# Performance work log

Hardware: AMD Instinct MI355X
Metric: run time of the kernel (lower is better)

The kernel has to match this reference:

```python
import jax, jax.numpy as jnp
import numpy as np

# Dimensions inferred from VSSBlockOneWay(hidden_dim=256, ssm_d_state=64, forward_type='m0_noz')
B_, L_, D_ = 8, 2048, 256      # batch, seq_len, d_model
DIN, N_, P_ = 512, 64, 64      # d_inner = 2*d_model, d_state, head_dim
H_ = DIN // P_                 # n_heads = 8


def _ln(x, w, b, eps=1e-5):
    m = x.mean(-1, keepdims=True)
    v = ((x - m) ** 2).mean(-1, keepdims=True)
    return (x - m) * jax.lax.rsqrt(v + eps) * w + b


def setup_inputs() -> dict:
    key = jax.random.key(0)
    ks = jax.random.split(key, 8)
    s = lambda k, shape, sc: jax.random.normal(k, shape, jnp.float32) * sc
    return dict(
        src=jax.random.normal(ks[0], (B_, L_, D_), jnp.float32),
        ln_w=jnp.ones((D_,), jnp.float32), ln_b=jnp.zeros((D_,), jnp.float32),
        W_in=s(ks[1], (D_, DIN), 0.02),
        conv_w=s(ks[2], (DIN, 1, 3), 0.1),            # depthwise conv1d kernel
        conv_b=jnp.zeros((DIN,), jnp.float32),
        W_xproj=s(ks[3], (DIN, H_ + 2 * N_), 0.02),   # -> (dt | B | C)
        dt_bias=s(ks[4], (H_,), 0.1),
        A_log=jnp.log(jnp.arange(1, H_ + 1, dtype=jnp.float32)),  # Mamba2 A-init
        Ds=jnp.ones((H_,), jnp.float32),
        oln_w=jnp.ones((DIN,), jnp.float32), oln_b=jnp.zeros((DIN,), jnp.float32),
        W_out=s(ks[5], (DIN, D_), 0.02),
    )


def reference(src, ln_w, ln_b, W_in, conv_w, conv_b, W_xproj, dt_bias,
              A_log, Ds, oln_w, oln_b, W_out):
    B, L, D = src.shape
    H, N, P = H_, N_, P_
    x = _ln(src, ln_w, ln_b)
    u = x @ W_in                                                    # (B,L,DIN)
    # depthwise conv over sequence, SAME padding (VMamba uses non-causal dwconv)
    uc = jax.lax.conv_general_dilated(
        u.transpose(0, 2, 1), conv_w, (1,), 'SAME',
        feature_group_count=DIN, dimension_numbers=('NCH', 'OIH', 'NCH'))
    u = jax.nn.gelu((uc + conv_b[None, :, None]).transpose(0, 2, 1),
                    approximate=False)                              # (B,L,DIN)
    dbc = u @ W_xproj                                               # (B,L,H+2N)
    dt = jax.nn.softplus(dbc[..., :H] + dt_bias)                    # (B,L,H)
    Bm = dbc[..., H:H + N]                                          # (B,L,N)
    Cm = dbc[..., H + N:]                                           # (B,L,N)
    A = -jnp.exp(A_log)                                             # (H,)
    decay = jnp.exp(dt * A)                                         # (B,L,H)
    xh = u.reshape(B, L, H, P)
    dtx = dt[..., None] * xh                                        # (B,L,H,P)

    def step(h, inp):
        dec_t, dtx_t, B_t, C_t = inp
        # h: (B,H,P,N)
        h = h * dec_t[:, :, None, None] + dtx_t[..., None] * B_t[:, None, None, :]
        y = jnp.einsum('bhpn,bn->bhp', h, C_t)
        return h, y

    h0 = jnp.zeros((B, H, P, N), u.dtype)
    inputs = (decay.transpose(1, 0, 2), dtx.transpose(1, 0, 2, 3),
              Bm.transpose(1, 0, 2), Cm.transpose(1, 0, 2))
    _, ys = jax.lax.scan(step, h0, inputs)                          # (L,B,H,P)
    y = ys.transpose(1, 0, 2, 3) + xh * Ds[None, None, :, None]
    y = _ln(y.reshape(B, L, DIN), oln_w, oln_b)
    # dropout / drop_path are identity at inference
    return src + y @ W_out
```

## Files before the change

### kernel.cpp

```cpp
#include <hip/hip_runtime.h>
#include <hip/hip_bf16.h>
#include <cmath>

typedef __hip_bfloat16 bf16;
typedef short bf16x8 __attribute__((ext_vector_type(8)));
typedef short bf16x4v __attribute__((ext_vector_type(4)));
typedef float f32x4 __attribute__((ext_vector_type(4)));

constexpr int B_ = 8, L_ = 2048, D_ = 256, DIN_ = 512;
constexpr int H_ = 8, N_ = 64, P_ = 64;
constexpr int BL_ = B_ * L_;
constexpr int NCH_ = 136;
constexpr int Q_ = 64;
constexpr int NC_ = L_ / Q_;

static __device__ __forceinline__ float b2f(bf16 x) { return __bfloat162float(x); }
static __device__ __forceinline__ bf16  f2b(float x) { return __float2bfloat16(x); }
static __device__ __forceinline__ bf16  rawb(short s) { __hip_bfloat16_raw r; r.x = (unsigned short)s; return (bf16)r; }
static __device__ __forceinline__ float sane(float v) { return (fabsf(v) <= 1e30f) ? v : 0.f; }
static __device__ __forceinline__ float loadx(const void* p, size_t i, bool isbf) {
    return isbf ? b2f(((const bf16*)p)[i]) : ((const float*)p)[i];
}
static __device__ __forceinline__ bf16x8 load8x(const void* p, size_t off, bool isbf) {
    if (isbf) return *(const bf16x8*)((const bf16*)p + off);
    const float4* fp = (const float4*)((const float*)p + off);
    float4 f0 = fp[0], f1 = fp[1];
    bf16 t[8] = {f2b(f0.x), f2b(f0.y), f2b(f0.z), f2b(f0.w),
                 f2b(f1.x), f2b(f1.y), f2b(f1.z), f2b(f1.w)};
    return *(bf16x8*)t;
}
static __device__ __forceinline__ int swz(int row, int col) { return col ^ (((row >> 3) & 7) * 8); }

static __device__ __forceinline__ f32x4 mfma16(bf16x8 a, bf16x8 b, f32x4 c) {
    return __builtin_amdgcn_mfma_f32_16x16x32_bf16(a, b, c, 0, 0, 0);
}
#define ONES8 bf16x8{16256, 16256, 16256, 16256, 16256, 16256, 16256, 16256}

__global__ __launch_bounds__(256) void prep_k(const void* __restrict__ Win, const void* __restrict__ Wx,
                       const void* __restrict__ Wo,
                       const void* __restrict__ ln_w, const void* __restrict__ ln_b,
                       const void* __restrict__ oln_w, const void* __restrict__ oln_b,
                       bf16* __restrict__ WinT, bf16* __restrict__ WxT, bf16* __restrict__ WoT,
                       float* __restrict__ colsum1, float* __restrict__ bias1,
                       float* __restrict__ colsum2, float* __restrict__ bias2,
                       const unsigned short* __restrict__ flagp) {
    const bool isbf = flagp[0] != 0;
    const int bx = blockIdx.x, tid = threadIdx.x;
    if (bx < 88) {
        __shared__ float T[64][65];
        if (bx < 32) {
            int d0 = (bx & 3) * 64, n0 = (bx >> 2) * 64;
#pragma unroll
            for (int i = 0; i < 16; i++) {
                int e = tid + 256 * i; int r = e >> 6, c = e & 63;
                T[r][c] = loadx(Win, (size_t)(d0 + r) * DIN_ + n0 + c, isbf);
            }
            __syncthreads();
#pragma unroll
            for (int i = 0; i < 16; i++) {
                int e = tid + 256 * i; int r = e >> 6, c = e & 63;
                WinT[(size_t)(n0 + r) * D_ + d0 + c] = f2b(loadx(ln_w, d0 + c, isbf) * T[c][r]);
            }
        } else if (bx < 64) {
            int t2 = bx - 32;
            int k0 = (t2 & 7) * 64, d0 = (t2 >> 3) * 64;
#pragma unroll
            for (int i = 0; i < 16; i++) {
                int e = tid + 256 * i; int r = e >> 6, c = e & 63;
                T[r][c] = loadx(Wo, (size_t)(k0 + r) * D_ + d0 + c, isbf);
            }
            __syncthreads();
#pragma unroll
            for (int i = 0; i < 16; i++) {
                int e = tid + 256 * i; int r = e >> 6, c = e & 63;
                WoT[(size_t)(d0 + r) * DIN_ + k0 + c] = f2b(loadx(oln_w, k0 + c, isbf) * T[c][r]);
            }
        } else {
            int t3 = bx - 64;
            int i0 = (t3 & 7) * 64, j0 = (t3 >> 3) * 64;
#pragma unroll
            for (int i = 0; i < 16; i++) {
                int e = tid + 256 * i; int r = e >> 6, c = e & 63;
                int j = j0 + c;
                T[r][c] = (j < NCH_) ? loadx(Wx, (size_t)(i0 + r) * NCH_ + j, isbf) : 0.f;
            }
            __syncthreads();
#pragma unroll
            for (int i = 0; i < 16; i++) {
                int e = tid + 256 * i; int r = e >> 6, c = e & 63;
                WxT[(size_t)(j0 + r) * DIN_ + i0 + c] = f2b(T[c][r]);
            }
        }
        return;
    }
    const int o = (bx - 88) * 4 + (tid >> 6);
    const int lane = tid & 63;
    float cs = 0.f, bs = 0.f;
    if (o < DIN_) {
        int n = o;
        for (int i = lane; i < D_; i += 64) {
            float wv = loadx(Win, (size_t)i * DIN_ + n, isbf);
            cs += loadx(ln_w, i, isbf) * wv;
            bs += loadx(ln_b, i, isbf) * wv;
        }
    } else {
        int d = o - DIN_;
        for (int k = lane; k < DIN_; k += 64) {
            float wv = loadx(Wo, (size_t)k * D_ + d, isbf);
            cs += loadx(oln_w, k, isbf) * wv;
            bs += loadx(oln_b, k, isbf) * wv;
        }
    }
#pragma unroll
    for (int off = 32; off >= 1; off >>= 1) { cs += __shfl_xor(cs, off); bs += __shfl_xor(bs, off); }
    if (lane == 0) {
        if (o < DIN_) { colsum1[o] = cs; bias1[o] = bs; }
        else          { colsum2[o - DIN_] = cs; bias2[o - DIN_] = bs; }
    }
}

__global__ __launch_bounds__(256) void gemm1_k(const void* __restrict__ src,
                                               const bf16* __restrict__ WinT,
                                               const float* __restrict__ colsum1,
                                               const float* __restrict__ bias1,
                                               bf16* __restrict__ u0,
                                               const unsigned short* __restrict__ flagp) {
    const bool isbf = flagp[0] != 0;
    constexpr int K = D_;
    constexpr int STR = K + 8;
    constexpr int CH = K / 8;
    __shared__ bf16 Blds[64 * STR];
    const int tid = threadIdx.x;
    const int n0 = blockIdx.y * 64;
#pragma unroll
    for (int i = 0; i < 64 * CH / 256; i++) {
        int e = tid + 256 * i;
        int r = e / CH, cch = e % CH;
        bf16x8 v = *(const bf16x8*)(WinT + (size_t)(n0 + r) * K + cch * 8);
        *(bf16x8*)(&Blds[r * STR + cch * 8]) = v;
    }
    __syncthreads();
    const int wave = tid >> 6, lane = tid & 63;
    const int quad = lane >> 4, l16 = lane & 15;
    const int m0 = blockIdx.x * 128 + wave * 32;
    const bf16x8 ones = ONES8;
    f32x4 acc[2][4], accS[2], accS2[2];
#pragma unroll
    for (int i = 0; i < 2; i++) {
        accS[i] = f32x4{0.f, 0.f, 0.f, 0.f};
        accS2[i] = f32x4{0.f, 0.f, 0.f, 0.f};
#pragma unroll
        for (int j = 0; j < 4; j++) acc[i][j] = f32x4{0.f, 0.f, 0.f, 0.f};
    }
    const size_t r0 = (size_t)(m0 + l16) * K + quad * 8;
    const size_t r1 = r0 + (size_t)16 * K;
#pragma unroll
    for (int k0 = 0; k0 < K; k0 += 32) {
        bf16x8 a0 = load8x(src, r0 + k0, isbf);
        bf16x8 a1 = load8x(src, r1 + k0, isbf);
        accS[0]  = mfma16(a0, ones, accS[0]);
        accS2[0] = mfma16(a0, a0, accS2[0]);
        accS[1]  = mfma16(a1, ones, accS[1]);
        accS2[1] = mfma16(a1, a1, accS2[1]);
#pragma unroll
        for (int i = 0; i < 4; i++) {
            bf16x8 bb = *(const bf16x8*)(&Blds[(16 * i + l16) * STR + k0 + quad * 8]);
            acc[0][i] = mfma16(a0, bb, acc[0][i]);
            acc[1][i] = mfma16(a1, bb, acc[1][i]);
        }
    }
    float cs[4], bsv[4];
#pragma unroll
    for (int i = 0; i < 4; i++) { int n = n0 + 16 * i + l16; cs[i] = colsum1[n]; bsv[i] = bias1[n]; }
#pragma unroll
    for (int rb = 0; rb < 2; rb++)
#pragma unroll
        for (int r = 0; r < 4; r++) {
            int rl = quad * 4 + r;
            float sv  = accS[rb][r];
            float s2v = __shfl(accS2[rb][r], (quad << 4) + rl);
            float mean = sv * (1.f / D_);
            float var  = s2v * (1.f / D_) - mean * mean;
            float rs = rsqrtf(fmaxf(var, 0.f) + 1e-5f);
            int m = m0 + rb * 16 + rl;
#pragma unroll
            for (int i = 0; i < 4; i++) {
                int n = n0 + 16 * i + l16;
                float v = rs * (acc[rb][i][r] - mean * cs[i]) + bsv[i];
                u0[(size_t)m * DIN_ + n] = f2b(v);
            }
        }
}

template<int MODE>
__global__ __launch_bounds__(256) void gemmB_k(const bf16* __restrict__ A,
                                               const bf16* __restrict__ BT,
                                               void* __restrict__ Cout,
                                               const void* __restrict__ resid,
                                               const float* __restrict__ colsum,
                                               const float* __restrict__ biasv,
                                               const void* __restrict__ dt_bias,
                                               const void* __restrict__ A_log,
                                               float* __restrict__ dtg,
                                               float* __restrict__ dtAg,
                                               const unsigned short* __restrict__ flagp) {
    const bool isbf = flagp[0] != 0;
    constexpr int K = 512;
    constexpr int KH = 256;
    constexpr int STR = KH + 8;
    constexpr int CH = KH / 8;
    __shared__ bf16 Blds[64 * STR];
    const int tid = threadIdx.x;
    const int n0 = blockIdx.y * 64;
    const int wave = tid >> 6, lane = tid & 63;
    const int quad = lane >> 4, l16 = lane & 15;
    const int m0 = blockIdx.x * 128 + wave * 32;
    const bf16x8 ones = ONES8;
    f32x4 acc[2][4], accS[2], accS2[2];
#pragma unroll
    for (int i = 0; i < 2; i++) {
        accS[i] = f32x4{0.f, 0.f, 0.f, 0.f};
        accS2[i] = f32x4{0.f, 0.f, 0.f, 0.f};
#pragma unroll
        for (int j = 0; j < 4; j++) acc[i][j] = f32x4{0.f, 0.f, 0.f, 0.f};
    }
    const bf16* a0p = A + (size_t)(m0 + l16) * K + quad * 8;
    const bf16* a1p = a0p + (size_t)16 * K;
#pragma unroll
    for (int kh = 0; kh < 2; kh++) {
        if (kh) __syncthreads();
#pragma unroll
        for (int i = 0; i < 64 * CH / 256; i++) {
            int e = tid + 256 * i;
            int r = e / CH, cch = e % CH;
            bf16x8 v = *(const bf16x8*)(BT + (size_t)(n0 + r) * K + kh * KH + cch * 8);
            *(bf16x8*)(&Blds[r * STR + cch * 8]) = v;
        }
        __syncthreads();
        const bf16* ah0 = a0p + kh * KH;
        const bf16* ah1 = a1p + kh * KH;
#pragma unroll 4
        for (int k0 = 0; k0 < KH; k0 += 32) {
            bf16x8 a0 = *(const bf16x8*)(ah0 + k0);
            bf16x8 a1 = *(const bf16x8*)(ah1 + k0);
            if (MODE == 1) {
                accS[0]  = mfma16(a0, ones, accS[0]);
                accS2[0] = mfma16(a0, a0, accS2[0]);
                accS[1]  = mfma16(a1, ones, accS[1]);
                accS2[1] = mfma16(a1, a1, accS2[1]);
            }
#pragma unroll
            for (int i = 0; i < 4; i++) {
                bf16x8 bb = *(const bf16x8*)(&Blds[(16 * i + l16) * STR + k0 + quad * 8]);
                acc[0][i] = mfma16(a0, bb, acc[0][i]);
                acc[1][i] = mfma16(a1, bb, acc[1][i]);
            }
        }
    }
    if (MODE == 0) {
#pragma unroll
        for (int rb = 0; rb < 2; rb++)
#pragma unroll
            for (int r = 0; r < 4; r++) {
                int m = m0 + rb * 16 + quad * 4 + r;
#pragma unroll
                for (int i = 0; i < 4; i++) {
                    int n = n0 + 16 * i + l16;
                    if (n < NCH_) ((bf16*)Cout)[(size_t)m * NCH_ + n] = f2b(acc[rb][i][r]);
                }
            }
        if (blockIdx.y == 0 && l16 < 8) {
            float bb = loadx(dt_bias, l16, isbf);
            float Ah = -__expf(fminf(loadx(A_log, l16, isbf), 30.f));
#pragma unroll
            for (int rb = 0; rb < 2; rb++)
#pragma unroll
                for (int r = 0; r < 4; r++) {
                    int m = m0 + rb * 16 + quad * 4 + r;
                    float raw = acc[rb][0][r] + bb;
                    float sp = raw > 20.f ? raw : log1pf(__expf(raw));
                    sp = fminf(sp, 60.f);
                    dtg[(size_t)m * H_ + l16]  = sp;
                    dtAg[(size_t)m * H_ + l16] = sp * Ah;
                }
        }
    } else {
        float cs[4], bsv[4];
#pragma unroll
        for (int i = 0; i < 4; i++) { int n = n0 + 16 * i + l16; cs[i] = colsum[n]; bsv[i] = biasv[n]; }
#pragma unroll
        for (int rb = 0; rb < 2; rb++)
#pragma unroll
            for (int r = 0; r < 4; r++) {
                int rl = quad * 4 + r;
                float sv  = accS[rb][r];
                float s2v = __shfl(accS2[rb][r], (quad << 4) + rl);
                float mean = sv * (1.f / K);
                float var  = s2v * (1.f / K) - mean * mean;
                float rs = rsqrtf(fmaxf(var, 0.f) + 1e-5f);
                int m = m0 + rb * 16 + rl;
#pragma unroll
                for (int i = 0; i < 4; i++) {
                    int n = n0 + 16 * i + l16;
                    size_t o = (size_t)m * D_ + n;
                    float v = rs * (acc[rb][i][r] - mean * cs[i]) + bsv[i] + loadx(resid, o, isbf);
                    v = sane(v);
                    if (isbf) ((bf16*)Cout)[o] = f2b(v);
                    else      ((float*)Cout)[o] = v;
                }
            }
    }
}

constexpr int CSTRIP_ = 4;
__global__ __launch_bounds__(256) void conv_k(const bf16* __restrict__ u0,
                                              const void* __restrict__ cw,
                                              const void* __restrict__ cb,
                                              bf16* __restrict__ u,
                                              const unsigned short* __restrict__ flagp) {
    const bool isbf = flagp[0] != 0;
    __shared__ float wlds[2048];
    {
        int t = threadIdx.x;
#pragma unroll
        for (int i = 0; i < 6; i++) { int e = t + 256 * i; wlds[e] = loadx(cw, e, isbf); }
        wlds[t + 1536] = loadx(cb, t, isbf);
        wlds[t + 1792] = loadx(cb, t + 256, isbf);
    }
    __syncthreads();
    const int wave = threadIdx.x >> 6, lane = threadIdx.x & 63;
    const int sid = blockIdx.x * 4 + wave;
    const int bl0 = sid * CSTRIP_;
    const int l0 = bl0 & (L_ - 1);
    const int c8 = lane * 8;
    float w0[8], w1[8], w2[8], bias[8];
#pragma unroll
    for (int t = 0; t < 8; t++) {
        int ch = c8 + t;
        w0[t] = wlds[ch * 3 + 0];
        w1[t] = wlds[ch * 3 + 1];
        w2[t] = wlds[ch * 3 + 2];
        bias[t] = wlds[1536 + ch];
    }
    const bf16x8* rp = (const bf16x8*)(u0 + (size_t)bl0 * DIN_ + c8);
    bf16x8 zero = {0, 0, 0, 0, 0, 0, 0, 0};
    bf16x8 vl = (l0 > 0) ? rp[-64] : zero;
    bf16x8 vm = rp[0];
#pragma unroll
    for (int i = 0; i < CSTRIP_; i++) {
        int l = l0 + i;
        bf16x8 vr = (l < L_ - 1) ? rp[64 * (i + 1)] : zero;
        bf16 ob[8];
#pragma unroll
        for (int t = 0; t < 8; t++) {
            float a = bias[t] + w1[t] * b2f(rawb(vm[t]))
                    + w0[t] * b2f(rawb(vl[t])) + w2[t] * b2f(rawb(vr[t]));
            float ge = 0.5f * a * (1.f + erff(a * 0.70710678118f));
            ob[t] = f2b(ge);
        }
        *(bf16x8*)(u + (size_t)(bl0 + i) * DIN_ + c8) = *(bf16x8*)ob;
        vl = vm; vm = vr;
    }
}

__global__ __launch_bounds__(256) void chunk_state_k(const bf16* __restrict__ ubuf,
                                                     const bf16* __restrict__ dbcb,
                                                     const float* __restrict__ dtg,
                                                     const float* __restrict__ dtAg,
                                                     bf16* __restrict__ HS,
                                                     float* __restrict__ cdg) {
    const int idx = blockIdx.x;
    const int c = idx & 31, h = (idx >> 5) & 7, b = idx >> 8;
    const int bh = b * 8 + h;
    const int blbase = b * L_ + c * Q_;
    __shared__ bf16 Xw[64][72];
    __shared__ bf16 BTb[64][72];
    const int tid = threadIdx.x;
    const int lane = tid & 63;
    float dA  = dtAg[(size_t)(blbase + lane) * H_ + h];
    float dtv = dtg[(size_t)(blbase + lane) * H_ + h];
    const int jr = tid >> 3, p8 = (tid & 7) * 8;
    bf16x8 xv0 = *(const bf16x8*)(ubuf + (size_t)(blbase + jr) * DIN_ + h * 64 + p8);
    bf16x8 bv0 = *(const bf16x8*)(dbcb + (size_t)(blbase + jr) * NCH_ + 8 + p8);
    bf16x8 xv1 = *(const bf16x8*)(ubuf + (size_t)(blbase + jr + 32) * DIN_ + h * 64 + p8);
    bf16x8 bv1 = *(const bf16x8*)(dbcb + (size_t)(blbase + jr + 32) * NCH_ + 8 + p8);
    float v = dA;
#pragma unroll
    for (int off = 1; off < 64; off <<= 1) { float t = __shfl_up(v, off); if (lane >= off) v += t; }
    float segEnd = __shfl(v, 63);
    float fjl = __expf(fminf(segEnd - v, 0.f)) * dtv;
    if (tid == 0) cdg[bh * NC_ + c] = __expf(fminf(segEnd, 0.f));
    float fs0 = __shfl(fjl, jr);
    float fs1 = __shfl(fjl, jr + 32);
#pragma unroll
    for (int t = 0; t < 8; t++) {
        int p = p8 + t;
        Xw[p][swz(p, jr)]       = f2b(fs0 * b2f(rawb(xv0[t])));
        BTb[p][swz(p, jr)]      = rawb(bv0[t]);
        Xw[p][swz(p, jr + 32)]  = f2b(fs1 * b2f(rawb(xv1[t])));
        BTb[p][swz(p, jr + 32)] = rawb(bv1[t]);
    }
    __syncthreads();
    const int wave = tid >> 6, quad = lane >> 4, l16 = lane & 15;
    const int p0 = wave * 16;
    f32x4 acc[4];
#pragma unroll
    for (int i = 0; i < 4; i++) acc[i] = f32x4{0.f, 0.f, 0.f, 0.f};
#pragma unroll
    for (int ks = 0; ks < 2; ks++) {
        int pa = p0 + l16;
        bf16x8 a = *(const bf16x8*)(&Xw[pa][swz(pa, ks * 32 + quad * 8)]);
#pragma unroll
        for (int nt = 0; nt < 4; nt++) {
            int nb = nt * 16 + l16;
            bf16x8 bb = *(const bf16x8*)(&BTb[nb][swz(nb, ks * 32 + quad * 8)]);
            acc[nt] = mfma16(a, bb, acc[nt]);
        }
    }
    size_t slot = (size_t)(bh * NC_ + c) * 4096;
#pragma unroll
    for (int nt = 0; nt < 4; nt++)
#pragma unroll
        for (int r = 0; r < 4; r++) {
            int p = p0 + quad * 4 + r, n = nt * 16 + l16;
            HS[slot + p * 64 + n] = f2b(sane(acc[nt][r]));
        }
}

__global__ __launch_bounds__(256) void chunk_rec_k(bf16* __restrict__ HS,
                                                   const float* __restrict__ cdg) {
    const int bh = blockIdx.x >> 2, sub = blockIdx.x & 3;
    const int eo = sub * 1024 + threadIdx.x * 4;
    bf16* base = HS + (size_t)bh * (NC_ * 4096) + eo;
    bf16x4v v[NC_];
#pragma unroll
    for (int c = 0; c < NC_; c++) v[c] = *(const bf16x4v*)(base + (size_t)c * 4096);
    float cdr[NC_];
#pragma unroll
    for (int c = 0; c < NC_; c++) cdr[c] = cdg[bh * NC_ + c];
    float h0 = 0.f, h1 = 0.f, h2 = 0.f, h3 = 0.f;
#pragma unroll
    for (int c = 0; c < NC_; c++) {
        bf16 ob[4] = {f2b(h0), f2b(h1), f2b(h2), f2b(h3)};
        *(bf16x4v*)(base + (size_t)c * 4096) = *(bf16x4v*)ob;
        float cd = cdr[c];
        h0 = cd * h0 + b2f(rawb(v[c][0]));
        h1 = cd * h1 + b2f(rawb(v[c][1]));
        h2 = cd * h2 + b2f(rawb(v[c][2]));
        h3 = cd * h3 + b2f(rawb(v[c][3]));
    }
}

__global__ __launch_bounds__(256) void chunk_out_k(bf16* __restrict__ ubuf,
                                                   const bf16* __restrict__ dbcb,
                                                   const float* __restrict__ dtg,
                                                   const float* __restrict__ dtAg,
                                                   const bf16* __restrict__ HS,
                                                   const void* __restrict__ Ds,
                                                   bf16* __restrict__ ybuf,
                                                   const unsigned short* __restrict__ flagp) {
    const bool isbf = flagp[0] != 0;
    const int idx = blockIdx.x;
    const int c = idx & 31, h = (idx >> 5) & 7, b = idx >> 8;
    const int bh = b * 8 + h;
    const int blbase = b * L_ + c * Q_;
    const size_t slotbase = (size_t)(bh * NC_ + c) * 4096;
    __shared__ bf16 Xb[64][72];
    __shared__ bf16 Gb[64][72];
    const int tid = threadIdx.x;
    const int lane = tid & 63;
    float dA  = dtAg[(size_t)(blbase + lane) * H_ + h];
    float dtl = dtg[(size_t)(blbase + lane) * H_ + h];
    const int rr = tid >> 3, k8 = (tid & 7) * 8;
    bf16x8 xva = *(const bf16x8*)(ubuf + (size_t)(blbase + rr) * DIN_ + h * 64 + k8);
    bf16x8 xvb = *(const bf16x8*)(ubuf + (size_t)(blbase + rr + 32) * DIN_ + h * 64 + k8);
    float segl = dA;
#pragma unroll
    for (int off = 1; off < 64; off <<= 1) { float t = __shfl_up(segl, off); if (lane >= off) segl += t; }
    float PLl = __expf(fminf(segl, 0.f));
#pragma unroll
    for (int t = 0; t < 8; t++) {
        int p = k8 + t;
        Xb[p][swz(p, rr)]      = rawb(xva[t]);
        Xb[p][swz(p, rr + 32)] = rawb(xvb[t]);
    }
    __syncthreads();
    const int wave = tid >> 6, quad = lane >> 4, l16 = lane & 15;
    const int l0 = wave * 16;
    f32x4 g[4];
#pragma unroll
    for (int i = 0; i < 4; i++) g[i] = f32x4{0.f, 0.f, 0.f, 0.f};
#pragma unroll
    for (int ks = 0; ks < 2; ks++) {
        bf16x8 a = *(const bf16x8*)(dbcb + (size_t)(blbase + l0 + l16) * NCH_ + 72 + ks * 32 + quad * 8);
#pragma unroll
        for (int jt = 0; jt < 4; jt++) {
            bf16x8 bb = *(const bf16x8*)(dbcb + (size_t)(blbase + jt * 16 + l16) * NCH_ + 8 + ks * 32 + quad * 8);
            g[jt] = mfma16(a, bb, g[jt]);
        }
    }
#pragma unroll
    for (int jt = 0; jt < 4; jt++) {
        int j = jt * 16 + l16;
        float segj = __shfl(segl, j);
        float dtj  = __shfl(dtl, j);
#pragma unroll
        for (int r = 0; r < 4; r++) {
            int l = l0 + quad * 4 + r;
            float e = __expf(fminf(__shfl(segl, l) - segj, 0.f));
            float gv = (j <= l) ? sane(g[jt][r]) * e * dtj : 0.f;
            Gb[l][swz(l, j)] = f2b(sane(gv));
        }
    }
    __syncthreads();
    f32x4 y1[4], y2[4];
#pragma unroll
    for (int i = 0; i < 4; i++) { y1[i] = f32x4{0.f, 0.f, 0.f, 0.f}; y2[i] = f32x4{0.f, 0.f, 0.f, 0.f}; }
#pragma unroll
    for (int ks = 0; ks < 2; ks++) {
        int la = l0 + l16;
        bf16x8 ag = *(const bf16x8*)(&Gb[la][swz(la, ks * 32 + quad * 8)]);
        bf16x8 ac = *(const bf16x8*)(dbcb + (size_t)(blbase + la) * NCH_ + 72 + ks * 32 + quad * 8);
#pragma unroll
        for (int pt = 0; pt < 4; pt++) {
            int pb = pt * 16 + l16;
            bf16x8 bx = *(const bf16x8*)(&Xb[pb][swz(pb, ks * 32 + quad * 8)]);
            bf16x8 bhf = *(const bf16x8*)(HS + slotbase + (size_t)pb * 64 + ks * 32 + quad * 8);
            y1[pt] = mfma16(ag, bx, y1[pt]);
            y2[pt] = mfma16(ac, bhf, y2[pt]);
        }
    }
    float dsH = loadx(Ds, h, isbf);
#pragma unroll
    for (int pt = 0; pt < 4; pt++) {
        int p = pt * 16 + l16;
#pragma unroll
        for (int r = 0; r < 4; r++) {
            int l = l0 + quad * 4 + r;
            float yv = y1[pt][r] + __shfl(PLl, l) * y2[pt][r] + dsH * b2f(Xb[p][swz(p, l)]);
            ybuf[(size_t)(blbase + l) * DIN_ + h * 64 + p] = f2b(sane(yv));
        }
    }
}

extern "C" void kernel_launch(void* const* d_in, const int* in_sizes, int n_in,
                              void* d_out, int out_size, void* d_ws, size_t ws_size,
                              hipStream_t stream) {
    const void* src     = d_in[0];
    const void* ln_w    = d_in[1];
    const void* ln_b    = d_in[2];
    const void* W_in    = d_in[3];
    const void* conv_w  = d_in[4];
    const void* conv_b  = d_in[5];
    const void* W_xproj = d_in[6];
    const void* dt_bias = d_in[7];
    const void* A_log   = d_in[8];
    const void* Ds      = d_in[9];
    const void* oln_w   = d_in[10];
    const void* oln_b   = d_in[11];
    const void* W_out   = d_in[12];
    const unsigned short* flagp = (const unsigned short*)ln_w;

    char* w = (char*)d_ws;
    size_t off = 0;
    auto alloc = [&](size_t bytes) { void* p = w + off; off += (bytes + 255) & ~(size_t)255; return p; };
    char*   regB   = (char*)alloc((size_t)BL_ * DIN_ * 2);
    char*   regC   = (char*)alloc((size_t)BL_ * DIN_ * 2);
    bf16*   dbcb   = (bf16*)alloc((size_t)BL_ * NCH_ * 2);
    float*  dtg    = (float*)alloc((size_t)BL_ * H_ * 4);
    float*  dtAg   = (float*)alloc((size_t)BL_ * H_ * 4);
    bf16*   WinT   = (bf16*)alloc((size_t)DIN_ * D_ * 2);
    bf16*   WxT    = (bf16*)alloc((size_t)192 * DIN_ * 2);
    bf16*   WoT    = (bf16*)alloc((size_t)D_ * DIN_ * 2);
    float*  colsum1= (float*)alloc(DIN_ * 4);
    float*  bias1  = (float*)alloc(DIN_ * 4);
    float*  colsum2= (float*)alloc(D_ * 4);
    float*  bias2  = (float*)alloc(D_ * 4);
    float*  cdg    = (float*)alloc((size_t)64 * NC_ * 4);

    bf16* u0buf = (bf16*)regB;
    bf16* HS    = (bf16*)regB;
    bf16* ubuf  = (bf16*)regC;
    bf16* ybuf  = (bf16*)regC;

    prep_k<<<88 + 192, 256, 0, stream>>>(W_in, W_xproj, W_out, ln_w, ln_b, oln_w, oln_b,
                                         WinT, WxT, WoT, colsum1, bias1, colsum2, bias2, flagp);
    gemm1_k<<<dim3(BL_ / 128, 8), 256, 0, stream>>>(src, WinT, colsum1, bias1, u0buf, flagp);
    conv_k<<<BL_ / CSTRIP_ / 4, 256, 0, stream>>>(u0buf, conv_w, conv_b, ubuf, flagp);
    gemmB_k<0><<<dim3(BL_ / 128, 3), 256, 0, stream>>>(ubuf, WxT, dbcb, nullptr, nullptr, nullptr,
                                                       dt_bias, A_log, dtg, dtAg, flagp);
    chunk_state_k<<<B_ * H_ * NC_, 256, 0, stream>>>(ubuf, dbcb, dtg, dtAg, HS, cdg);
    chunk_rec_k<<<256, 256, 0, stream>>>(HS, cdg);
    chunk_out_k<<<B_ * H_ * NC_, 256, 0, stream>>>(ubuf, dbcb, dtg, dtAg, HS, Ds, ybuf, flagp);
    gemmB_k<1><<<dim3(BL_ / 128, 4), 256, 0, stream>>>(ybuf, WoT, d_out, src, colsum2, bias2,
                                                       nullptr, nullptr, nullptr, nullptr, flagp);
}
```

Baseline: 200.6 us.

## Split B/C projections into aligned buffers and prefetch GEMM A-operand rows

The packed dt|B|C buffer with a 136-element row stride is replaced by two separate 64-wide bf16 buffers for B and C, so the chunk kernels read them with aligned, contiguous 128-byte rows. In gemm1_k and gemmB_k, all A-operand loads for a K-half are issued into registers up front, or software-pipelined for the fp32 input path, instead of being interleaved with the MFMAs. chunk_out_k also loads its C fragments once and reuses them in both phases. This raises register pressure and may lower occupancy in the GEMM kernels.

```diff
diff --git a/kernel.cpp b/kernel.cpp
--- a/kernel.cpp
+++ b/kernel.cpp
@@ -21,10 +21,7 @@
 static __device__ __forceinline__ float loadx(const void* p, size_t i, bool isbf) {
     return isbf ? b2f(((const bf16*)p)[i]) : ((const float*)p)[i];
 }
-static __device__ __forceinline__ bf16x8 load8x(const void* p, size_t off, bool isbf) {
-    if (isbf) return *(const bf16x8*)((const bf16*)p + off);
-    const float4* fp = (const float4*)((const float*)p + off);
-    float4 f0 = fp[0], f1 = fp[1];
+static __device__ __forceinline__ bf16x8 packf(float4 f0, float4 f1) {
     bf16 t[8] = {f2b(f0.x), f2b(f0.y), f2b(f0.z), f2b(f0.w),
                  f2b(f1.x), f2b(f1.y), f2b(f1.z), f2b(f1.w)};
     return *(bf16x8*)t;
@@ -154,10 +151,7 @@
     }
     const size_t r0 = (size_t)(m0 + l16) * K + quad * 8;
     const size_t r1 = r0 + (size_t)16 * K;
-#pragma unroll
-    for (int k0 = 0; k0 < K; k0 += 32) {
-        bf16x8 a0 = load8x(src, r0 + k0, isbf);
-        bf16x8 a1 = load8x(src, r1 + k0, isbf);
+    auto domfma = [&](bf16x8 a0, bf16x8 a1, int k0) {
         accS[0]  = mfma16(a0, ones, accS[0]);
         accS2[0] = mfma16(a0, a0, accS2[0]);
         accS[1]  = mfma16(a1, ones, accS[1]);
@@ -167,6 +161,37 @@
             bf16x8 bb = *(const bf16x8*)(&Blds[(16 * i + l16) * STR + k0 + quad * 8]);
             acc[0][i] = mfma16(a0, bb, acc[0][i]);
             acc[1][i] = mfma16(a1, bb, acc[1][i]);
+        }
+    };
+    if (isbf) {
+        const bf16* s0 = (const bf16*)src + r0;
+        const bf16* s1 = (const bf16*)src + r1;
+        bf16x8 pa0[8], pa1[8];
+#pragma unroll
+        for (int s = 0; s < 8; s++) {
+            pa0[s] = *(const bf16x8*)(s0 + s * 32);
+            pa1[s] = *(const bf16x8*)(s1 + s * 32);
+        }
+#pragma unroll
+        for (int s = 0; s < 8; s++) domfma(pa0[s], pa1[s], s * 32);
+    } else {
+        const float* s0 = (const float*)src + r0;
+        const float* s1 = (const float*)src + r1;
+        float4 c00 = *(const float4*)(s0);
+        float4 c01 = *(const float4*)(s0 + 4);
+        float4 c10 = *(const float4*)(s1);
+        float4 c11 = *(const float4*)(s1 + 4);
+#pragma unroll
+        for (int s = 0; s < 8; s++) {
+            float4 n00, n01, n10, n11;
+            if (s < 7) {
+                n00 = *(const float4*)(s0 + (s + 1) * 32);
+                n01 = *(const float4*)(s0 + (s + 1) * 32 + 4);
+                n10 = *(const float4*)(s1 + (s + 1) * 32);
+                n11 = *(const float4*)(s1 + (s + 1) * 32 + 4);
+            }
+            domfma(packf(c00, c01), packf(c10, c11), s * 32);
+            if (s < 7) { c00 = n00; c01 = n01; c10 = n10; c11 = n11; }
         }
     }
     float cs[4], bsv[4];
@@ -196,6 +221,8 @@
 __global__ __launch_bounds__(256) void gemmB_k(const bf16* __restrict__ A,
                                                const bf16* __restrict__ BT,
                                                void* __restrict__ Cout,
+                                               bf16* __restrict__ Bmb,
+                                               bf16* __restrict__ Cmb,
                                                const void* __restrict__ resid,
                                                const float* __restrict__ colsum,
                                                const float* __restrict__ biasv,
@@ -228,6 +255,14 @@
     const bf16* a1p = a0p + (size_t)16 * K;
 #pragma unroll
     for (int kh = 0; kh < 2; kh++) {
+        const bf16* ah0 = a0p + kh * KH;
+        const bf16* ah1 = a1p + kh * KH;
+        bf16x8 pa0[8], pa1[8];
+#pragma unroll
+        for (int s = 0; s < 8; s++) {
+            pa0[s] = *(const bf16x8*)(ah0 + s * 32);
+            pa1[s] = *(const bf16x8*)(ah1 + s * 32);
+        }
         if (kh) __syncthreads();
 #pragma unroll
         for (int i = 0; i < 64 * CH / 256; i++) {
@@ -237,12 +272,10 @@
             *(bf16x8*)(&Blds[r * STR + cch * 8]) = v;
         }
         __syncthreads();
-        const bf16* ah0 = a0p + kh * KH;
-        const bf16* ah1 = a1p + kh * KH;
-#pragma unroll 4
-        for (int k0 = 0; k0 < KH; k0 += 32) {
-            bf16x8 a0 = *(const bf16x8*)(ah0 + k0);
-            bf16x8 a1 = *(const bf16x8*)(ah1 + k0);
+#pragma unroll
+        for (int s = 0; s < 8; s++) {
+            int k0 = s * 32;
+            bf16x8 a0 = pa0[s], a1 = pa1[s];
             if (MODE == 1) {
                 accS[0]  = mfma16(a0, ones, accS[0]);
                 accS2[0] = mfma16(a0, a0, accS2[0]);
@@ -266,7 +299,9 @@
 #pragma unroll
                 for (int i = 0; i < 4; i++) {
                     int n = n0 + 16 * i + l16;
-                    if (n < NCH_) ((bf16*)Cout)[(size_t)m * NCH_ + n] = f2b(acc[rb][i][r]);
+                    bf16 val = f2b(acc[rb][i][r]);
+                    if (n >= 8 && n < 72)        Bmb[(size_t)m * 64 + (n - 8)]  = val;
+                    else if (n >= 72 && n < NCH_) Cmb[(size_t)m * 64 + (n - 72)] = val;
                 }
             }
         if (blockIdx.y == 0 && l16 < 8) {
@@ -364,7 +399,7 @@
 }
 
 __global__ __launch_bounds__(256) void chunk_state_k(const bf16* __restrict__ ubuf,
-                                                     const bf16* __restrict__ dbcb,
+                                                     const bf16* __restrict__ Bmb,
                                                      const float* __restrict__ dtg,
                                                      const float* __restrict__ dtAg,
                                                      bf16* __restrict__ HS,
@@ -381,9 +416,9 @@
     float dtv = dtg[(size_t)(blbase + lane) * H_ + h];
     const int jr = tid >> 3, p8 = (tid & 7) * 8;
     bf16x8 xv0 = *(const bf16x8*)(ubuf + (size_t)(blbase + jr) * DIN_ + h * 64 + p8);
-    bf16x8 bv0 = *(const bf16x8*)(dbcb + (size_t)(blbase + jr) * NCH_ + 8 + p8);
+    bf16x8 bv0 = *(const bf16x8*)(Bmb + (size_t)(blbase + jr) * 64 + p8);
     bf16x8 xv1 = *(const bf16x8*)(ubuf + (size_t)(blbase + jr + 32) * DIN_ + h * 64 + p8);
-    bf16x8 bv1 = *(const bf16x8*)(dbcb + (size_t)(blbase + jr + 32) * NCH_ + 8 + p8);
+    bf16x8 bv1 = *(const bf16x8*)(Bmb + (size_t)(blbase + jr + 32) * 64 + p8);
     float v = dA;
 #pragma unroll
     for (int off = 1; off < 64; off <<= 1) { float t = __shfl_up(v, off); if (lane >= off) v += t; }
@@ -452,7 +487,8 @@
 }
 
 __global__ __launch_bounds__(256) void chunk_out_k(bf16* __restrict__ ubuf,
-                                                   const bf16* __restrict__ dbcb,
+                                                   const bf16* __restrict__ Bmb,
+                                                   const bf16* __restrict__ Cmb,
                                                    const float* __restrict__ dtg,
                                                    const float* __restrict__ dtAg,
                                                    const bf16* __restrict__ HS,
@@ -487,16 +523,20 @@
     __syncthreads();
     const int wave = tid >> 6, quad = lane >> 4, l16 = lane & 15;
     const int l0 = wave * 16;
+    const int la = l0 + l16;
+    bf16x8 ac[2];
+#pragma unroll
+    for (int ks = 0; ks < 2; ks++)
+        ac[ks] = *(const bf16x8*)(Cmb + (size_t)(blbase + la) * 64 + ks * 32 + quad * 8);
     f32x4 g[4];
 #pragma unroll
     for (int i = 0; i < 4; i++) g[i] = f32x4{0.f, 0.f, 0.f, 0.f};
 #pragma unroll
     for (int ks = 0; ks < 2; ks++) {
-        bf16x8 a = *(const bf16x8*)(dbcb + (size_t)(blbase + l0 + l16) * NCH_ + 72 + ks * 32 + quad * 8);
 #pragma unroll
         for (int jt = 0; jt < 4; jt++) {
-            bf16x8 bb = *(const bf16x8*)(dbcb + (size_t)(blbase + jt * 16 + l16) * NCH_ + 8 + ks * 32 + quad * 8);
-            g[jt] = mfma16(a, bb, g[jt]);
+            bf16x8 bb = *(const bf16x8*)(Bmb + (size_t)(blbase + jt * 16 + l16) * 64 + ks * 32 + quad * 8);
+            g[jt] = mfma16(ac[ks], bb, g[jt]);
         }
     }
 #pragma unroll
@@ -518,16 +558,14 @@
     for (int i = 0; i < 4; i++) { y1[i] = f32x4{0.f, 0.f, 0.f, 0.f}; y2[i] = f32x4{0.f, 0.f, 0.f, 0.f}; }
 #pragma unroll
     for (int ks = 0; ks < 2; ks++) {
-        int la = l0 + l16;
         bf16x8 ag = *(const bf16x8*)(&Gb[la][swz(la, ks * 32 + quad * 8)]);
-        bf16x8 ac = *(const bf16x8*)(dbcb + (size_t)(blbase + la) * NCH_ + 72 + ks * 32 + quad * 8);
 #pragma unroll
         for (int pt = 0; pt < 4; pt++) {
             int pb = pt * 16 + l16;
             bf16x8 bx = *(const bf16x8*)(&Xb[pb][swz(pb, ks * 32 + quad * 8)]);
             bf16x8 bhf = *(const bf16x8*)(HS + slotbase + (size_t)pb * 64 + ks * 32 + quad * 8);
             y1[pt] = mfma16(ag, bx, y1[pt]);
-            y2[pt] = mfma16(ac, bhf, y2[pt]);
+            y2[pt] = mfma16(ac[ks], bhf, y2[pt]);
         }
     }
     float dsH = loadx(Ds, h, isbf);
@@ -566,7 +604,8 @@
     auto alloc = [&](size_t bytes) { void* p = w + off; off += (bytes + 255) & ~(size_t)255; return p; };
     char*   regB   = (char*)alloc((size_t)BL_ * DIN_ * 2);
     char*   regC   = (char*)alloc((size_t)BL_ * DIN_ * 2);
-    bf16*   dbcb   = (bf16*)alloc((size_t)BL_ * NCH_ * 2);
+    bf16*   Bmb    = (bf16*)alloc((size_t)BL_ * 64 * 2);
+    bf16*   Cmb    = (bf16*)alloc((size_t)BL_ * 64 * 2);
     float*  dtg    = (float*)alloc((size_t)BL_ * H_ * 4);
     float*  dtAg   = (float*)alloc((size_t)BL_ * H_ * 4);
     bf16*   WinT   = (bf16*)alloc((size_t)DIN_ * D_ * 2);
@@ -587,11 +626,13 @@
                                          WinT, WxT, WoT, colsum1, bias1, colsum2, bias2, flagp);
     gemm1_k<<<dim3(BL_ / 128, 8), 256, 0, stream>>>(src, WinT, colsum1, bias1, u0buf, flagp);
     conv_k<<<BL_ / CSTRIP_ / 4, 256, 0, stream>>>(u0buf, conv_w, conv_b, ubuf, flagp);
-    gemmB_k<0><<<dim3(BL_ / 128, 3), 256, 0, stream>>>(ubuf, WxT, dbcb, nullptr, nullptr, nullptr,
-                                                       dt_bias, A_log, dtg, dtAg, flagp);
-    chunk_state_k<<<B_ * H_ * NC_, 256, 0, stream>>>(ubuf, dbcb, dtg, dtAg, HS, cdg);
+    gemmB_k<0><<<dim3(BL_ / 128, 3), 256, 0, stream>>>(ubuf, WxT, nullptr, Bmb, Cmb, nullptr,
+                                                       nullptr, nullptr, dt_bias, A_log,
+                                                       dtg, dtAg, flagp);
+    chunk_state_k<<<B_ * H_ * NC_, 256, 0, stream>>>(ubuf, Bmb, dtg, dtAg, HS, cdg);
     chunk_rec_k<<<256, 256, 0, stream>>>(HS, cdg);
-    chunk_out_k<<<B_ * H_ * NC_, 256, 0, stream>>>(ubuf, dbcb, dtg, dtAg, HS, Ds, ybuf, flagp);
-    gemmB_k<1><<<dim3(BL_ / 128, 4), 256, 0, stream>>>(ybuf, WoT, d_out, src, colsum2, bias2,
-                                                       nullptr, nullptr, nullptr, nullptr, flagp);
-}
+    chunk_out_k<<<B_ * H_ * NC_, 256, 0, stream>>>(ubuf, Bmb, Cmb, dtg, dtAg, HS, Ds, ybuf, flagp);
+    gemmB_k<1><<<dim3(BL_ / 128, 4), 256, 0, stream>>>(ybuf, WoT, d_out, nullptr, nullptr, src,
+                                                       colsum2, bias2, nullptr, nullptr,
+                                                       nullptr, nullptr, flagp);
+}
```

New measurement: 206.8 us. 3.1% more time.

## Keep gemm1 A rows in registers and loop over four N tiles per block

Applied to the files above, without the earlier changes.

gemm1 now loads each wave's 32 source rows (full K=256) into registers once, computes the LayerNorm statistics once, then iterates over four 64-column weight tiles staged through LDS. The grid shrinks from 8 to 2 column groups. This cuts redundant global reads and fp32-to-bf16 conversion of src and repeated stat MFMAs by 4x. In exchange it uses more registers, serialises tile loads with extra barriers, and launches fewer blocks.

```diff
diff --git a/kernel.cpp b/kernel.cpp
--- a/kernel.cpp
+++ b/kernel.cpp
@@ -21,10 +21,7 @@
 static __device__ __forceinline__ float loadx(const void* p, size_t i, bool isbf) {
     return isbf ? b2f(((const bf16*)p)[i]) : ((const float*)p)[i];
 }
-static __device__ __forceinline__ bf16x8 load8x(const void* p, size_t off, bool isbf) {
-    if (isbf) return *(const bf16x8*)((const bf16*)p + off);
-    const float4* fp = (const float4*)((const float*)p + off);
-    float4 f0 = fp[0], f1 = fp[1];
+static __device__ __forceinline__ bf16x8 packf(float4 f0, float4 f1) {
     bf16 t[8] = {f2b(f0.x), f2b(f0.y), f2b(f0.z), f2b(f0.w),
                  f2b(f1.x), f2b(f1.y), f2b(f1.z), f2b(f1.w)};
     return *(bf16x8*)t;
@@ -131,47 +128,45 @@
     constexpr int CH = K / 8;
     __shared__ bf16 Blds[64 * STR];
     const int tid = threadIdx.x;
-    const int n0 = blockIdx.y * 64;
-#pragma unroll
-    for (int i = 0; i < 64 * CH / 256; i++) {
-        int e = tid + 256 * i;
-        int r = e / CH, cch = e % CH;
-        bf16x8 v = *(const bf16x8*)(WinT + (size_t)(n0 + r) * K + cch * 8);
-        *(bf16x8*)(&Blds[r * STR + cch * 8]) = v;
-    }
-    __syncthreads();
+    const int nhalf = blockIdx.y * 256;
     const int wave = tid >> 6, lane = tid & 63;
     const int quad = lane >> 4, l16 = lane & 15;
     const int m0 = blockIdx.x * 128 + wave * 32;
     const bf16x8 ones = ONES8;
-    f32x4 acc[2][4], accS[2], accS2[2];
+    const size_t r0 = (size_t)(m0 + l16) * K + quad * 8;
+    const size_t r1 = r0 + (size_t)16 * K;
+    bf16x8 pa0[8], pa1[8];
+    if (isbf) {
+        const bf16* s0 = (const bf16*)src + r0;
+        const bf16* s1 = (const bf16*)src + r1;
+#pragma unroll
+        for (int s = 0; s < 8; s++) {
+            pa0[s] = *(const bf16x8*)(s0 + s * 32);
+            pa1[s] = *(const bf16x8*)(s1 + s * 32);
+        }
+    } else {
+        const float* s0 = (const float*)src + r0;
+        const float* s1 = (const float*)src + r1;
+#pragma unroll
+        for (int s = 0; s < 8; s++) {
+            pa0[s] = packf(*(const float4*)(s0 + s * 32), *(const float4*)(s0 + s * 32 + 4));
+            pa1[s] = packf(*(const float4*)(s1 + s * 32), *(const float4*)(s1 + s * 32 + 4));
+        }
+    }
+    f32x4 accS[2], accS2[2];
 #pragma unroll
     for (int i = 0; i < 2; i++) {
         accS[i] = f32x4{0.f, 0.f, 0.f, 0.f};
         accS2[i] = f32x4{0.f, 0.f, 0.f, 0.f};
-#pragma unroll
-        for (int j = 0; j < 4; j++) acc[i][j] = f32x4{0.f, 0.f, 0.f, 0.f};
-    }
-    const size_t r0 = (size_t)(m0 + l16) * K + quad * 8;
-    const size_t r1 = r0 + (size_t)16 * K;
-#pragma unroll
-    for (int k0 = 0; k0 < K; k0 += 32) {
-        bf16x8 a0 = load8x(src, r0 + k0, isbf);
-        bf16x8 a1 = load8x(src, r1 + k0, isbf);
-        accS[0]  = mfma16(a0, ones, accS[0]);
-        accS2[0] = mfma16(a0, a0, accS2[0]);
-        accS[1]  = mfma16(a1, ones, accS[1]);
-        accS2[1] = mfma16(a1, a1, accS2[1]);
-#pragma unroll
-        for (int i = 0; i < 4; i++) {
-            bf16x8 bb = *(const bf16x8*)(&Blds[(16 * i + l16) * STR + k0 + quad * 8]);
-            acc[0][i] = mfma16(a0, bb, acc[0][i]);
-            acc[1][i] = mfma16(a1, bb, acc[1][i]);
-        }
-    }
-    float cs[4], bsv[4];
-#pragma unroll
-    for (int i = 0; i < 4; i++) { int n = n0 + 16 * i + l16; cs[i] = colsum1[n]; bsv[i] = bias1[n]; }
+    }
+#pragma unroll
+    for (int s = 0; s < 8; s++) {
+        accS[0]  = mfma16(pa0[s], ones, accS[0]);
+        accS2[0] = mfma16(pa0[s], pa0[s], accS2[0]);
+        accS[1]  = mfma16(pa1[s], ones, accS[1]);
+        accS2[1] = mfma16(pa1[s], pa1[s], accS2[1]);
+    }
+    float meanv[2][4], rsv[2][4];
 #pragma unroll
     for (int rb = 0; rb < 2; rb++)
 #pragma unroll
@@ -181,15 +176,53 @@
             float s2v = __shfl(accS2[rb][r], (quad << 4) + rl);
             float mean = sv * (1.f / D_);
             float var  = s2v * (1.f / D_) - mean * mean;
-            float rs = rsqrtf(fmaxf(var, 0.f) + 1e-5f);
-            int m = m0 + rb * 16 + rl;
+            meanv[rb][r] = mean;
+            rsv[rb][r] = rsqrtf(fmaxf(var, 0.f) + 1e-5f);
+        }
+#pragma unroll 1
+    for (int nt = 0; nt < 4; nt++) {
+        const int n0 = nhalf + nt * 64;
+        if (nt) __syncthreads();
+#pragma unroll
+        for (int i = 0; i < 64 * CH / 256; i++) {
+            int e = tid + 256 * i;
+            int r = e / CH, cch = e % CH;
+            bf16x8 v = *(const bf16x8*)(WinT + (size_t)(n0 + r) * K + cch * 8);
+            *(bf16x8*)(&Blds[r * STR + cch * 8]) = v;
+        }
+        __syncthreads();
+        f32x4 acc[2][4];
+#pragma unroll
+        for (int i = 0; i < 2; i++)
+#pragma unroll
+            for (int j = 0; j < 4; j++) acc[i][j] = f32x4{0.f, 0.f, 0.f, 0.f};
+#pragma unroll
+        for (int s = 0; s < 8; s++) {
+            int k0 = s * 32;
 #pragma unroll
             for (int i = 0; i < 4; i++) {
-                int n = n0 + 16 * i + l16;
-                float v = rs * (acc[rb][i][r] - mean * cs[i]) + bsv[i];
-                u0[(size_t)m * DIN_ + n] = f2b(v);
-            }
-        }
+                bf16x8 bb = *(const bf16x8*)(&Blds[(16 * i + l16) * STR + k0 + quad * 8]);
+                acc[0][i] = mfma16(pa0[s], bb, acc[0][i]);
+                acc[1][i] = mfma16(pa1[s], bb, acc[1][i]);
+            }
+        }
+        float cs[4], bsv[4];
+#pragma unroll
+        for (int i = 0; i < 4; i++) { int n = n0 + 16 * i + l16; cs[i] = colsum1[n]; bsv[i] = bias1[n]; }
+#pragma unroll
+        for (int rb = 0; rb < 2; rb++)
+#pragma unroll
+            for (int r = 0; r < 4; r++) {
+                int rl = quad * 4 + r;
+                int m = m0 + rb * 16 + rl;
+#pragma unroll
+                for (int i = 0; i < 4; i++) {
+                    int n = n0 + 16 * i + l16;
+                    float v = rsv[rb][r] * (acc[rb][i][r] - meanv[rb][r] * cs[i]) + bsv[i];
+                    u0[(size_t)m * DIN_ + n] = f2b(v);
+                }
+            }
+    }
 }
 
 template<int MODE>
@@ -585,7 +618,7 @@
 
     prep_k<<<88 + 192, 256, 0, stream>>>(W_in, W_xproj, W_out, ln_w, ln_b, oln_w, oln_b,
                                          WinT, WxT, WoT, colsum1, bias1, colsum2, bias2, flagp);
-    gemm1_k<<<dim3(BL_ / 128, 8), 256, 0, stream>>>(src, WinT, colsum1, bias1, u0buf, flagp);
+    gemm1_k<<<dim3(BL_ / 128, 2), 256, 0, stream>>>(src, WinT, colsum1, bias1, u0buf, flagp);
     conv_k<<<BL_ / CSTRIP_ / 4, 256, 0, stream>>>(u0buf, conv_w, conv_b, ubuf, flagp);
     gemmB_k<0><<<dim3(BL_ / 128, 3), 256, 0, stream>>>(ubuf, WxT, dbcb, nullptr, nullptr, nullptr,
                                                        dt_bias, A_log, dtg, dtAg, flagp);
```

Result: no change. 202.6 us (+1.0%).
